# Performance work log

Measured on AMD Instinct MI355X. Metric: run time of the kernel, lower is better.

The kernel has to match this reference:

```python
import jax, jax.numpy as jnp
import numpy as np

B, S, SE, H, NH = 1, 2048, 2048, 1024, 16
HD = H // NH
INNER = 4 * H
EPS = 1e-5


def layer_norm(x, g, b):
    mu = jnp.mean(x, axis=-1, keepdims=True)
    var = jnp.mean(jnp.square(x - mu), axis=-1, keepdims=True)
    return (x - mu) * jax.lax.rsqrt(var + EPS) * g + b


def split_heads(x):  # [B,T,H] -> [B,NH,T,HD]
    b, t, _ = x.shape
    return x.reshape(b, t, NH, HD).transpose(0, 2, 1, 3)


def merge_heads(x):  # [B,NH,T,HD] -> [B,T,H]
    b, nh, t, hd = x.shape
    return x.transpose(0, 2, 1, 3).reshape(b, t, nh * hd)


def setup_inputs() -> dict:
    key = jax.random.key(0)
    ks = jax.random.split(key, 16)
    n = lambda k, shp: (jax.random.normal(k, shp, jnp.float32) * 0.02)
    return {
        "hidden_states": jax.random.normal(ks[0], (B, S, H), jnp.float32),
        "encoder_hidden_states": jax.random.normal(ks[1], (B, SE, H), jnp.float32),
        "scorer_logits": jax.random.normal(ks[2], (B, SE), jnp.float32),
        "ln1_g": jnp.ones((H,), jnp.float32), "ln1_b": jnp.zeros((H,), jnp.float32),
        "c_attn_w": n(ks[3], (H, 3 * H)), "c_attn_b": jnp.zeros((3 * H,), jnp.float32),
        "attn_proj_w": n(ks[4], (H, H)), "attn_proj_b": jnp.zeros((H,), jnp.float32),
        "lnx_g": jnp.ones((H,), jnp.float32), "lnx_b": jnp.zeros((H,), jnp.float32),
        "q_attn_w": n(ks[5], (H, H)), "q_attn_b": jnp.zeros((H,), jnp.float32),
        "x_kv_w": n(ks[6], (H, 2 * H)), "x_kv_b": jnp.zeros((2 * H,), jnp.float32),
        "x_proj_w": n(ks[7], (H, H)), "x_proj_b": jnp.zeros((H,), jnp.float32),
        "ln2_g": jnp.ones((H,), jnp.float32), "ln2_b": jnp.zeros((H,), jnp.float32),
        "fc_w": n(ks[8], (H, INNER)), "fc_b": jnp.zeros((INNER,), jnp.float32),
        "mlp_proj_w": n(ks[9], (INNER, H)), "mlp_proj_b": jnp.zeros((H,), jnp.float32),
    }


def _attn_core(q, k, v, extra_bias=None, causal_bool=False, tril_diag2_additive=False):
    # q,k,v: [B,NH,T,HD]; eager attention, materializes full score matrix (faithful to source)
    w = jnp.einsum("bhqd,bhkd->bhqk", q, k) / jnp.sqrt(jnp.asarray(HD, q.dtype))
    ql, kl = q.shape[-2], k.shape[-2]
    neg = jnp.finfo(w.dtype).min
    if causal_bool:
        mask = jnp.tril(jnp.ones((ql, kl), bool))  # self-attn boolean causal mask
        w = jnp.where(mask[None, None], w, neg)
    if tril_diag2_additive:
        cm = jnp.tril(jnp.ones((ql, kl), w.dtype), k=2)  # limit_cross_attn: tril diagonal=2
        w = w + jnp.where(cm == 0, neg, jnp.zeros((), w.dtype))[None, None]
    if extra_bias is not None:
        w = w + extra_bias[:, None, None, :]  # scorer_logits additive per-key bias
    w = jax.nn.softmax(w, axis=-1)
    return jnp.einsum("bhqk,bhkd->bhqd", w, v)


def reference(hidden_states, encoder_hidden_states, scorer_logits,
              ln1_g, ln1_b, c_attn_w, c_attn_b, attn_proj_w, attn_proj_b,
              lnx_g, lnx_b, q_attn_w, q_attn_b, x_kv_w, x_kv_b, x_proj_w, x_proj_b,
              ln2_g, ln2_b, fc_w, fc_b, mlp_proj_w, mlp_proj_b):
    # --- self attention ---
    residual = hidden_states
    x = layer_norm(hidden_states, ln1_g, ln1_b)
    qkv = x @ c_attn_w + c_attn_b
    q, k, v = jnp.split(qkv, 3, axis=-1)
    a = _attn_core(split_heads(q), split_heads(k), split_heads(v), causal_bool=True)
    a = merge_heads(a) @ attn_proj_w + attn_proj_b
    hidden_states = a + residual
    # --- cross attention (limit_cross_attn=True, scorer_logits bias) ---
    residual = hidden_states
    x = layer_norm(hidden_states, lnx_g, lnx_b)
    q = x @ q_attn_w + q_attn_b
    kv = encoder_hidden_states @ x_kv_w + x_kv_b
    k, v = jnp.split(kv, 2, axis=-1)
    a = _attn_core(split_heads(q), split_heads(k), split_heads(v),
                   extra_bias=scorer_logits, tril_diag2_additive=True)
    a = merge_heads(a) @ x_proj_w + x_proj_b
    hidden_states = residual + a
    # --- MLP (gelu_new = tanh approx) ---
    residual = hidden_states
    x = layer_norm(hidden_states, ln2_g, ln2_b)
    h = jax.nn.gelu(x @ fc_w + fc_b, approximate=True)
    hidden_states = residual + (h @ mlp_proj_w + mlp_proj_b)
    return hidden_states
```

## Files before the change

kernel.cpp:

```cpp
#include <hip/hip_runtime.h>
#include <stdint.h>

#define H     1024
#define S     2048
#define SEQE  2048
#define NHEAD 16
#define HD    64
#define INNER 4096
#define EPSLN 1e-5f
#define LOG2E 1.44269504089f
#define SCALE2 (0.125f * LOG2E)

typedef __attribute__((ext_vector_type(8))) short short8;
typedef __attribute__((ext_vector_type(4))) float floatx4;

__device__ __forceinline__ float b2f(unsigned short u){
  union { unsigned int i; float f; } v; v.i = ((unsigned int)u) << 16; return v.f;
}
__device__ __forceinline__ unsigned short f2b(float f){
  union { float f; unsigned int i; } v; v.f = f;
  unsigned int x = v.i;
  unsigned int r = (x + 0x7FFFu + ((x >> 16) & 1u)) >> 16;
  return (unsigned short)r;
}
__device__ __forceinline__ float fexp2(float x){ return __builtin_amdgcn_exp2f(x); }
__device__ __forceinline__ float gelu_tanh(float x){
  float x3 = x*x*x;
  float t = tanhf(0.7978845608028654f*(x + 0.044715f*x3));
  return 0.5f*x*(1.0f+t);
}

__device__ __forceinline__ void gld16(const unsigned short* g, unsigned short* l){
  __builtin_amdgcn_global_load_lds(
      (const __attribute__((address_space(1))) unsigned int*)g,
      (__attribute__((address_space(3))) unsigned int*)l,
      16, 0, 0);
}

__global__ __launch_bounds__(256) void k_sniff(
    const unsigned short* __restrict__ p, int* __restrict__ flag){
  __shared__ int any;
  if (threadIdx.x == 0) any = 0;
  __syncthreads();
  int bad = 0;
  for (int i = threadIdx.x; i < 8192; i += 256){
    float v = b2f(p[i]);
    if (!(fabsf(v) < 1e6f)) bad = 1;
  }
  if (bad) any = 1;
  __syncthreads();
  if (threadIdx.x == 0) flag[0] = any;
}

struct PrepT {
  const void* src[7];
  unsigned short* dst[7];
  int R[7], C[7];
  int pre[8];
};
__global__ __launch_bounds__(256) void k_prep_t(PrepT d, const int* __restrict__ flag){
  __shared__ unsigned short t[32][33];
  int b = blockIdx.x;
  int m = 0;
  while (b >= d.pre[m+1]) m++;
  int ti = b - d.pre[m];
  int R = d.R[m], C = d.C[m];
  int tx = threadIdx.x & 31, ty = threadIdx.x >> 5;
  int tilesx = C >> 5;
  int bc = (ti % tilesx) << 5, br = (ti / tilesx) << 5;
  const float* sf = (const float*)d.src[m];
  const unsigned short* sb = (const unsigned short*)d.src[m];
  unsigned short* dst = d.dst[m];
  int fl = flag[0];
  #pragma unroll
  for (int i = 0; i < 4; i++){
    size_t idx = (size_t)(br + ty + i*8) * C + bc + tx;
    t[ty + i*8][tx] = fl ? f2b(sf[idx]) : sb[idx];
  }
  __syncthreads();
  #pragma unroll
  for (int i = 0; i < 4; i++)
    dst[(size_t)(bc + ty + i*8) * R + br + tx] = t[tx][ty + i*8];
}

struct SmallCvt {
  const void* src[16];
  unsigned short* dst[16];
  int n[16];
};
__global__ __launch_bounds__(256) void k_prep_c(
    const void* __restrict__ enc, unsigned short* __restrict__ enc_c,
    const void* __restrict__ hsv, float* __restrict__ hidden,
    SmallCvt sc, const int* __restrict__ flag){
  int b = blockIdx.x, tid = threadIdx.x;
  int fl = flag[0];
  if (b < 8192){
    int i = b*256 + tid;
    enc_c[i] = fl ? f2b(((const float*)enc)[i]) : ((const unsigned short*)enc)[i];
  } else if (b < 16384){
    int i = (b - 8192)*256 + tid;
    hidden[i] = fl ? ((const float*)hsv)[i] : b2f(((const unsigned short*)hsv)[i]);
  } else {
    int t = b - 16384;
    const float* sf = (const float*)sc.src[t];
    const unsigned short* sb = (const unsigned short*)sc.src[t];
    unsigned short* d = sc.dst[t];
    for (int i = tid; i < sc.n[t]; i += 256){
      float vv = fl ? sf[i] : b2f(sb[i]);
      if (t == 13) vv *= LOG2E;
      d[i] = f2b(vv);
    }
  }
}

__global__ __launch_bounds__(256) void k_layernorm(
    const float* __restrict__ x,
    const unsigned short* __restrict__ g, const unsigned short* __restrict__ bb,
    unsigned short* __restrict__ y){
  __shared__ float scratch[4];
  int row = blockIdx.x, tid = threadIdx.x;
  float v[4];
  #pragma unroll
  for (int i=0;i<4;i++) v[i] = x[(size_t)row*H + tid + i*256];
  float s = v[0]+v[1]+v[2]+v[3];
  for (int o=32;o;o>>=1) s += __shfl_xor(s,o,64);
  int wid = tid>>6, lane = tid&63;
  if (lane==0) scratch[wid]=s;
  __syncthreads();
  float mu = (scratch[0]+scratch[1]+scratch[2]+scratch[3]) * (1.0f/H);
  __syncthreads();
  float q = 0.f;
  #pragma unroll
  for (int i=0;i<4;i++){ float d=v[i]-mu; q += d*d; }
  for (int o=32;o;o>>=1) q += __shfl_xor(q,o,64);
  if (lane==0) scratch[wid]=q;
  __syncthreads();
  float var = (scratch[0]+scratch[1]+scratch[2]+scratch[3]) * (1.0f/H);
  float rstd = rsqrtf(var + EPSLN);
  #pragma unroll
  for (int i=0;i<4;i++){
    int idx = tid + i*256;
    float o = (v[i]-mu)*rstd*b2f(g[idx]) + b2f(bb[idx]);
    y[(size_t)row*H + idx] = f2b(o);
  }
}

__global__ __launch_bounds__(256) void k_gemm64(
    const unsigned short* __restrict__ A, const unsigned short* __restrict__ BT,
    const unsigned short* __restrict__ bias,
    unsigned short* __restrict__ outb, float* __restrict__ resid,
    int M, int N, int K, int mode, const int* __restrict__ flag,
    int vcol0, unsigned short* __restrict__ vtout)
{
  __shared__ __align__(16) unsigned short As[2][64*64];
  __shared__ __align__(16) unsigned short Bs[2][128*64];
  int tid = threadIdx.x;
  int bm0 = blockIdx.y * 64, bn0 = blockIdx.x * 128;
  int wid = tid >> 6, lane = tid & 63;
  int wm = (wid & 1) * 32, wn = (wid >> 1) * 64;
  floatx4 acc[2][4] = {};

  const unsigned short* gp[6];
  int lofs[6];
  int aseg[6];
  int lrow = lane >> 3, lchunk = (lane & 7) ^ lrow;
  #pragma unroll
  for (int t = 0; t < 6; t++){
    int seg = wid * 6 + t;
    if (seg < 8){
      gp[t] = A + (size_t)(bm0 + seg*8 + lrow) * K + lchunk*8;
      lofs[t] = seg * 512;
      aseg[t] = 1;
    } else {
      int s = seg - 8;
      gp[t] = BT + (size_t)(bn0 + s*8 + lrow) * K + lchunk*8;
      lofs[t] = s * 512;
      aseg[t] = 0;
    }
  }

  #pragma unroll
  for (int t = 0; t < 6; t++)
    gld16(gp[t], (aseg[t] ? As[0] : Bs[0]) + lofs[t]);

  int mrow = lane & 15, quad = lane >> 4;
  int ib = 0;
  for (int kt = 0; kt < K; kt += 64, ib ^= 1){
    __syncthreads();
    if (kt + 64 < K){
      #pragma unroll
      for (int t = 0; t < 6; t++)
        gld16(gp[t] + kt + 64, (aseg[t] ? As[ib^1] : Bs[ib^1]) + lofs[t]);
    }
    const unsigned short* Ac = As[ib];
    const unsigned short* Bc = Bs[ib];
    #pragma unroll
    for (int k2 = 0; k2 < 2; k2++){
      short8 af[2], bf[4];
      #pragma unroll
      for (int i = 0; i < 2; i++){
        int r = wm + i*16 + mrow;
        int slot = (k2*4 + quad) ^ (r & 7);
        af[i] = *(const short8*)&Ac[r*64 + slot*8];
      }
      #pragma unroll
      for (int j = 0; j < 4; j++){
        int r = wn + j*16 + mrow;
        int slot = (k2*4 + quad) ^ (r & 7);
        bf[j] = *(const short8*)&Bc[r*64 + slot*8];
      }
      #pragma unroll
      for (int i = 0; i < 2; i++){
        #pragma unroll
        for (int j = 0; j < 4; j++){
          acc[i][j] = __builtin_amdgcn_mfma_f32_16x16x32_bf16(af[i], bf[j], acc[i][j], 0,0,0);
        }
      }
    }
  }

  int colb = mrow, rowb = quad * 4;
  #pragma unroll
  for (int i=0;i<2;i++){
    #pragma unroll
    for (int j=0;j<4;j++){
      int col = bn0 + wn + j*16 + colb;
      float bv = b2f(bias[col]);
      int row0 = bm0 + wm + i*16 + rowb;
      if (mode == 4 && col >= vcol0){
        ushort4 uv;
        uv.x = f2b(acc[i][j][0] + bv);
        uv.y = f2b(acc[i][j][1] + bv);
        uv.z = f2b(acc[i][j][2] + bv);
        uv.w = f2b(acc[i][j][3] + bv);
        *(ushort4*)(vtout + (size_t)(col - vcol0)*M + row0) = uv;
      } else {
        #pragma unroll
        for (int rr=0;rr<4;rr++){
          int row = row0 + rr;
          float v = acc[i][j][rr] + bv;
          size_t off = (size_t)row*N + col;
          if      (mode == 0 || mode == 4){ outb[off] = f2b(v); }
          else if (mode == 1){ outb[off] = f2b(gelu_tanh(v)); }
          else               { resid[off] += v; }
        }
      }
    }
  }
}

__global__ __launch_bounds__(256) void k_gemm64s(
    const unsigned short* __restrict__ A, const unsigned short* __restrict__ BT,
    const unsigned short* __restrict__ bias,
    unsigned short* __restrict__ outb, float* __restrict__ resid,
    int M, int N, int K, int klen, int mode)
{
  __shared__ __align__(16) unsigned short As[2][64*64];
  __shared__ __align__(16) unsigned short Bs[2][64*64];
  int tid = threadIdx.x;
  int bm0 = blockIdx.y * 64, bn0 = blockIdx.x * 64;
  int k0 = blockIdx.z * klen;
  int wid = tid >> 6, lane = tid & 63;
  int wm = wid * 16;
  floatx4 acc[4] = {};

  const unsigned short* gp[4];
  int lofs[4];
  int aseg[4];
  int lrow = lane >> 3, lchunk = (lane & 7) ^ lrow;
  #pragma unroll
  for (int t = 0; t < 4; t++){
    int seg = wid * 4 + t;
    if (seg < 8){
      gp[t] = A + (size_t)(bm0 + seg*8 + lrow) * K + k0 + lchunk*8;
      lofs[t] = seg * 512;
      aseg[t] = 1;
    } else {
      int s = seg - 8;
      gp[t] = BT + (size_t)(bn0 + s*8 + lrow) * K + k0 + lchunk*8;
      lofs[t] = s * 512;
      aseg[t] = 0;
    }
  }

  #pragma unroll
  for (int t = 0; t < 4; t++)
    gld16(gp[t], (aseg[t] ? As[0] : Bs[0]) + lofs[t]);

  int mrow = lane & 15, quad = lane >> 4;
  int ib = 0;
  for (int kt = 0; kt < klen; kt += 64, ib ^= 1){
    __syncthreads();
    if (kt + 64 < klen){
      #pragma unroll
      for (int t = 0; t < 4; t++)
        gld16(gp[t] + kt + 64, (aseg[t] ? As[ib^1] : Bs[ib^1]) + lofs[t]);
    }
    const unsigned short* Ac = As[ib];
    const unsigned short* Bc = Bs[ib];
    #pragma unroll
    for (int k2 = 0; k2 < 2; k2++){
      short8 af, bf[4];
      {
        int r = wm + mrow;
        int slot = (k2*4 + quad) ^ (r & 7);
        af = *(const short8*)&Ac[r*64 + slot*8];
      }
      #pragma unroll
      for (int j = 0; j < 4; j++){
        int r = j*16 + mrow;
        int slot = (k2*4 + quad) ^ (r & 7);
        bf[j] = *(const short8*)&Bc[r*64 + slot*8];
      }
      #pragma unroll
      for (int j = 0; j < 4; j++)
        acc[j] = __builtin_amdgcn_mfma_f32_16x16x32_bf16(af, bf[j], acc[j], 0,0,0);
    }
  }

  int colb = mrow, rowb = quad * 4;
  #pragma unroll
  for (int j=0;j<4;j++){
    int col = bn0 + j*16 + colb;
    float bv = (blockIdx.z == 0) ? b2f(bias[col]) : 0.f;
    int row0 = bm0 + wm + rowb;
    #pragma unroll
    for (int rr=0;rr<4;rr++){
      int row = row0 + rr;
      float v = acc[j][rr] + bv;
      size_t off = (size_t)row*N + col;
      if (mode == 0) outb[off] = f2b(v);
      else           atomicAdd(&resid[off], v);
    }
  }
}

__global__ __launch_bounds__(256) void k_final(
    const float* __restrict__ hidden, unsigned short* __restrict__ out,
    const int* __restrict__ flag){
  int i = blockIdx.x * 256 + threadIdx.x;
  float v = hidden[i];
  if (flag[0]) ((float*)out)[i] = v;
  else         out[i] = f2b(v);
}

template<int CA, int SCOR>
__global__ __launch_bounds__(256) void k_flash2(
    const unsigned short* __restrict__ qb, int qstride,
    const unsigned short* __restrict__ kb, int kstride,
    const unsigned short* __restrict__ vt,
    const unsigned short* __restrict__ scorer,
    unsigned short* __restrict__ obuf, float* __restrict__ mlbuf, int TOTS)
{
  int t = blockIdx.x, h = blockIdx.y, sp = blockIdx.z;
  int klmax0 = 64*t + 64 + CA; if (klmax0 > S) klmax0 = S;
  int nch = (klmax0 + 63) >> 6;
  int nsp = (nch + 7) >> 3;
  if (sp >= nsp) return;
  int base = 0;
  for (int i = 0; i < t; i++){
    int km = 64*i + 64 + CA; if (km > S) km = S;
    base += (((km + 63) >> 6) + 7) >> 3;
  }
  int pidx = h*TOTS + base + sp;
  int c0 = sp*8, c1 = c0 + 8; if (c1 > nch) c1 = nch;

  __shared__ __align__(16) unsigned short Ks[2][64*64];
  __shared__ __align__(16) unsigned short VTs[64*64];
  __shared__ __align__(16) unsigned short Ps[4][16*72];
  __shared__ float scs[2][64];
  int tid = threadIdx.x;
  int q0 = t*64;
  int w = tid >> 6, lane = tid & 63;
  int cn = lane & 15, quad = lane >> 4, kq = quad * 8;
  unsigned short* Pw = Ps[w];
  int srow0 = w*16;
  int lr = lane >> 3;
  int lc = ((lane & 7) ^ lr) * 8;
  const unsigned short* kg0 = kb + (size_t)(srow0 + lr) * kstride + h*HD + lc;
  const unsigned short* kg1 = kb + (size_t)(srow0 + 8 + lr) * kstride + h*HD + lc;
  const unsigned short* vg0 = vt + (size_t)(h*HD + srow0 + lr) * S + lc;
  const unsigned short* vg1 = vt + (size_t)(h*HD + srow0 + 8 + lr) * S + lc;

  const unsigned short* qrow = qb + (size_t)(q0 + w*16 + cn) * qstride + h*HD;
  short8 qf0 = *(const short8*)(qrow + kq);
  short8 qf1 = *(const short8*)(qrow + kq + 32);
  floatx4 oacc[4] = {};
  float l_lane[4] = {0,0,0,0};
  float m_w = -1.0e38f;
  int qmr = q0 + w*16 + quad*4;

  {
    int kc = c0 * 64;
    gld16(kg0 + (size_t)kc * kstride, Ks[0] + srow0*64);
    gld16(kg1 + (size_t)kc * kstride, Ks[0] + (srow0 + 8)*64);
    if (SCOR && tid < 64) scs[0][tid] = b2f(scorer[kc + tid]);
  }

  int ib = 0;
  for (int ci = c0; ci < c1; ci++, ib ^= 1){
    int kc = ci * 64;
    __syncthreads();
    gld16(vg0 + kc, VTs + srow0*64);
    gld16(vg1 + kc, VTs + (srow0 + 8)*64);
    if (ci + 1 < c1){
      int kn2 = (ci + 1) * 64;
      gld16(kg0 + (size_t)kn2 * kstride, Ks[ib^1] + srow0*64);
      gld16(kg1 + (size_t)kn2 * kstride, Ks[ib^1] + (srow0 + 8)*64);
      if (SCOR && tid < 64) scs[ib^1][tid] = b2f(scorer[kn2 + tid]);
    }
    const unsigned short* Kc = Ks[ib];
    const float* scc = scs[ib];

    floatx4 sv[4] = {};
    #pragma unroll
    for (int t4=0;t4<4;t4++){
      int rr = t4*16 + cn;
      int s0 = ((quad    ) ^ (rr & 7)) * 8;
      int s1 = ((quad + 4) ^ (rr & 7)) * 8;
      short8 b0 = *(const short8*)&Kc[rr*64 + s0];
      short8 b1 = *(const short8*)&Kc[rr*64 + s1];
      sv[t4] = __builtin_amdgcn_mfma_f32_16x16x32_bf16(qf0, b0, sv[t4], 0,0,0);
      sv[t4] = __builtin_amdgcn_mfma_f32_16x16x32_bf16(qf1, b1, sv[t4], 0,0,0);
    }

    float vals[16];
    float lmax = -1.0e38f;
    if (kc + 63 > q0 + w*16 + CA){
      #pragma unroll
      for (int t4=0;t4<4;t4++){
        #pragma unroll
        for (int r=0;r<4;r++){
          float s = sv[t4][r] * SCALE2;
          if (SCOR) s += scc[t4*16 + cn];
          int kn = kc + t4*16 + cn;
          s = (kn <= qmr + r + CA) ? s : -1.0e38f;
          vals[t4*4+r] = s;
          lmax = fmaxf(lmax, s);
        }
      }
    } else {
      #pragma unroll
      for (int t4=0;t4<4;t4++){
        #pragma unroll
        for (int r=0;r<4;r++){
          float s = sv[t4][r] * SCALE2;
          if (SCOR) s += scc[t4*16 + cn];
          vals[t4*4+r] = s;
          lmax = fmaxf(lmax, s);
        }
      }
    }
    lmax = fmaxf(lmax, __shfl_xor(lmax,1,64));
    lmax = fmaxf(lmax, __shfl_xor(lmax,2,64));
    lmax = fmaxf(lmax, __shfl_xor(lmax,4,64));
    lmax = fmaxf(lmax, __shfl_xor(lmax,8,64));
    float mnew = fmaxf(m_w, lmax);
    float al = fexp2(m_w - mnew);
    m_w = mnew;
    #pragma unroll
    for (int r=0;r<4;r++) l_lane[r] *= al;
    #pragma unroll
    for (int t2=0;t2<4;t2++){
      #pragma unroll
      for (int r=0;r<4;r++) oacc[t2][r] *= al;
    }
    #pragma unroll
    for (int t4=0;t4<4;t4++){
      #pragma unroll
      for (int r=0;r<4;r++){
        float e = fexp2(vals[t4*4+r] - m_w);
        l_lane[r] += e;
        Pw[(quad*4+r)*72 + t4*16 + cn] = f2b(e);
      }
    }
    __syncthreads();
    short8 pf0 = *(const short8*)&Pw[cn*72 + kq];
    short8 pf1 = *(const short8*)&Pw[cn*72 + kq + 32];
    #pragma unroll
    for (int t2=0;t2<4;t2++){
      int rr = t2*16 + cn;
      int s0 = ((quad    ) ^ (rr & 7)) * 8;
      int s1 = ((quad + 4) ^ (rr & 7)) * 8;
      short8 v0 = *(const short8*)&VTs[rr*64 + s0];
      short8 v1 = *(const short8*)&VTs[rr*64 + s1];
      oacc[t2] = __builtin_amdgcn_mfma_f32_16x16x32_bf16(pf0, v0, oacc[t2], 0,0,0);
      oacc[t2] = __builtin_amdgcn_mfma_f32_16x16x32_bf16(pf1, v1, oacc[t2], 0,0,0);
    }
  }

  float lrow[4];
  #pragma unroll
  for (int r=0;r<4;r++){
    float l = l_lane[r];
    l += __shfl_xor(l,1,64); l += __shfl_xor(l,2,64);
    l += __shfl_xor(l,4,64); l += __shfl_xor(l,8,64);
    lrow[r] = l;
  }
  size_t ob = (size_t)pidx*4096 + (size_t)(w*16 + quad*4)*64;
  #pragma unroll
  for (int t2=0;t2<4;t2++){
    #pragma unroll
    for (int r=0;r<4;r++)
      obuf[ob + r*64 + t2*16 + cn] = f2b(oacc[t2][r]);
  }
  if (cn == 0){
    #pragma unroll
    for (int r=0;r<4;r++){
      int row64 = w*16 + quad*4 + r;
      mlbuf[((size_t)pidx*64 + row64)*2]   = m_w;
      mlbuf[((size_t)pidx*64 + row64)*2+1] = lrow[r];
    }
  }
}

template<int CA>
__global__ __launch_bounds__(256) void k_comb(
    const unsigned short* __restrict__ obuf, const float* __restrict__ mlbuf,
    unsigned short* __restrict__ out, int TOTS)
{
  int h = blockIdx.y;
  int row = blockIdx.x*16 + (threadIdx.x >> 4);
  int d0 = (threadIdx.x & 15) * 4;
  int t = row >> 6;
  int klmax0 = 64*t + 64 + CA; if (klmax0 > S) klmax0 = S;
  int nch = (klmax0 + 63) >> 6;
  int nsp = (nch + 7) >> 3;
  int base = 0;
  for (int i = 0; i < t; i++){
    int km = 64*i + 64 + CA; if (km > S) km = S;
    base += (((km + 63) >> 6) + 7) >> 3;
  }
  int row64 = row & 63;
  float mp[4], lp[4];
  float M = -1.0e38f;
  for (int p = 0; p < nsp; p++){
    int pi = h*TOTS + base + p;
    mp[p] = mlbuf[((size_t)pi*64 + row64)*2];
    lp[p] = mlbuf[((size_t)pi*64 + row64)*2+1];
    M = fmaxf(M, mp[p]);
  }
  float L = 0.f;
  float o0=0.f,o1=0.f,o2=0.f,o3=0.f;
  for (int p = 0; p < nsp; p++){
    int pi = h*TOTS + base + p;
    float wgt = fexp2(mp[p] - M);
    L += lp[p]*wgt;
    const unsigned short* op = obuf + (size_t)pi*4096 + row64*64 + d0;
    o0 += b2f(op[0])*wgt; o1 += b2f(op[1])*wgt;
    o2 += b2f(op[2])*wgt; o3 += b2f(op[3])*wgt;
  }
  float inv = 1.0f / L;
  size_t oo = (size_t)row*H + h*HD + d0;
  out[oo]   = f2b(o0*inv); out[oo+1] = f2b(o1*inv);
  out[oo+2] = f2b(o2*inv); out[oo+3] = f2b(o3*inv);
}

extern "C" void kernel_launch(void* const* d_in, const int* in_sizes, int n_in,
                              void* d_out, int out_size, void* d_ws, size_t ws_size,
                              hipStream_t stream)
{
  const void* hs          = d_in[0];
  const void* enc         = d_in[1];
  const void* scorer      = d_in[2];
  const void* ln1_g       = d_in[3];
  const void* ln1_b       = d_in[4];
  const void* c_attn_w    = d_in[5];
  const void* c_attn_b    = d_in[6];
  const void* attn_proj_w = d_in[7];
  const void* attn_proj_b = d_in[8];
  const void* lnx_g       = d_in[9];
  const void* lnx_b       = d_in[10];
  const void* q_attn_w    = d_in[11];
  const void* q_attn_b    = d_in[12];
  const void* x_kv_w      = d_in[13];
  const void* x_kv_b      = d_in[14];
  const void* x_proj_w    = d_in[15];
  const void* x_proj_b    = d_in[16];
  const void* ln2_g       = d_in[17];
  const void* ln2_b       = d_in[18];
  const void* fc_w        = d_in[19];
  const void* fc_b        = d_in[20];
  const void* mlp_proj_w  = d_in[21];
  const void* mlp_proj_b  = d_in[22];
  unsigned short* out = (unsigned short*)d_out;

  char* ws = (char*)d_ws; size_t off = 0;
  auto alloc = [&](size_t bytes)->void*{
    void* p = ws + off; off += (bytes + 255) & ~(size_t)255; return p;
  };
  unsigned short* wT_cattn = (unsigned short*)alloc((size_t)3072*1024*2);
  unsigned short* wT_aproj = (unsigned short*)alloc((size_t)1024*1024*2);
  unsigned short* wT_qattn = (unsigned short*)alloc((size_t)1024*1024*2);
  unsigned short* wT_xkv   = (unsigned short*)alloc((size_t)2048*1024*2);
  unsigned short* wT_xproj = (unsigned short*)alloc((size_t)1024*1024*2);
  unsigned short* wT_fc    = (unsigned short*)alloc((size_t)4096*1024*2);
  unsigned short* wT_mlp   = (unsigned short*)alloc((size_t)1024*4096*2);
  unsigned short* enc_c    = (unsigned short*)alloc((size_t)SEQE*H*2);
  unsigned short* canon    = (unsigned short*)alloc((size_t)32768*2);
  unsigned short* xln      = (unsigned short*)alloc((size_t)S*H*2);
  unsigned short* qkv      = (unsigned short*)alloc((size_t)S*3*H*2);
  unsigned short* attnout  = (unsigned short*)alloc((size_t)S*H*2);
  unsigned short* q2       = (unsigned short*)alloc((size_t)S*H*2);
  unsigned short* kvbuf    = (unsigned short*)alloc((size_t)SEQE*2*H*2);
  unsigned short* vt_self  = (unsigned short*)alloc((size_t)H*S*2);
  unsigned short* vt_cross = (unsigned short*)alloc((size_t)H*SEQE*2);
  unsigned short* fcbuf    = (unsigned short*)alloc((size_t)S*INNER*2);
  float*          hidden   = (float*)alloc((size_t)S*H*4);
  int*            flag     = (int*)alloc(256);

  unsigned short* obuf  = fcbuf;
  float*          mlbuf = (float*)(fcbuf + (size_t)16*83*4096);

  unsigned short* p = canon;
  auto carve = [&](int n)->unsigned short*{ unsigned short* q = p; p += n; return q; };
  unsigned short* c_ln1g = carve(1024); unsigned short* c_ln1b = carve(1024);
  unsigned short* c_catb = carve(3072); unsigned short* c_aprb = carve(1024);
  unsigned short* c_lnxg = carve(1024); unsigned short* c_lnxb = carve(1024);
  unsigned short* c_qatb = carve(1024); unsigned short* c_xkvb = carve(2048);
  unsigned short* c_xprb = carve(1024); unsigned short* c_ln2g = carve(1024);
  unsigned short* c_ln2b = carve(1024); unsigned short* c_fcb  = carve(4096);
  unsigned short* c_mlpb = carve(1024); unsigned short* c_scor = carve(2048);

  k_sniff<<<1, 256, 0, stream>>>((const unsigned short*)hs, flag);

  PrepT pt{};
  const void* tsrc[7] = {c_attn_w, attn_proj_w, q_attn_w, x_kv_w, x_proj_w, fc_w, mlp_proj_w};
  unsigned short* tdst[7] = {wT_cattn, wT_aproj, wT_qattn, wT_xkv, wT_xproj, wT_fc, wT_mlp};
  int tR[7] = {1024,1024,1024,1024,1024,1024,4096};
  int tC[7] = {3072,1024,1024,2048,1024,4096,1024};
  int acc_t = 0;
  for (int i=0;i<7;i++){
    pt.src[i]=tsrc[i]; pt.dst[i]=tdst[i]; pt.R[i]=tR[i]; pt.C[i]=tC[i];
    pt.pre[i]=acc_t; acc_t += (tC[i]>>5)*(tR[i]>>5);
  }
  pt.pre[7]=acc_t;
  k_prep_t<<<acc_t, 256, 0, stream>>>(pt, flag);

  SmallCvt sc{};
  const void* ssrc[14] = {ln1_g, ln1_b, c_attn_b, attn_proj_b, lnx_g, lnx_b,
                          q_attn_b, x_kv_b, x_proj_b, ln2_g, ln2_b, fc_b,
                          mlp_proj_b, scorer};
  unsigned short* sdst[14] = {c_ln1g, c_ln1b, c_catb, c_aprb, c_lnxg, c_lnxb,
                              c_qatb, c_xkvb, c_xprb, c_ln2g, c_ln2b, c_fcb,
                              c_mlpb, c_scor};
  int sn[14] = {1024,1024,3072,1024,1024,1024,1024,2048,1024,1024,1024,4096,1024,2048};
  for (int i=0;i<14;i++){ sc.src[i]=ssrc[i]; sc.dst[i]=sdst[i]; sc.n[i]=sn[i]; }
  k_prep_c<<<16384 + 14, 256, 0, stream>>>(enc, enc_c, hs, hidden, sc, flag);

  k_layernorm<<<S, 256, 0, stream>>>(hidden, c_ln1g, c_ln1b, xln);
  k_gemm64<<<dim3(3072/128, S/64), 256, 0, stream>>>(xln, wT_cattn, c_catb,
      qkv, nullptr, S, 3072, 1024, 4, flag, 2048, vt_self);
  k_flash2<0,0><<<dim3(32, NHEAD, 4), 256, 0, stream>>>(
      qkv, 3*H, qkv + 1024, 3*H, vt_self, nullptr, obuf, mlbuf, 80);
  k_comb<0><<<dim3(S/16, NHEAD), 256, 0, stream>>>(obuf, mlbuf, attnout, 80);
  k_gemm64s<<<dim3(1024/64, S/64, 2), 256, 0, stream>>>(attnout, wT_aproj, c_aprb,
      nullptr, hidden, S, 1024, 1024, 512, 2);

  k_layernorm<<<S, 256, 0, stream>>>(hidden, c_lnxg, c_lnxb, xln);
  k_gemm64s<<<dim3(1024/64, S/64, 1), 256, 0, stream>>>(xln, wT_qattn, c_qatb,
      q2, nullptr, S, 1024, 1024, 1024, 0);
  k_gemm64<<<dim3(2048/128, SEQE/64), 256, 0, stream>>>(enc_c, wT_xkv, c_xkvb,
      kvbuf, nullptr, SEQE, 2048, 1024, 4, flag, 1024, vt_cross);
  k_flash2<2,1><<<dim3(32, NHEAD, 4), 256, 0, stream>>>(
      q2, H, kvbuf, 2*H, vt_cross, c_scor, obuf, mlbuf, 83);
  k_comb<2><<<dim3(S/16, NHEAD), 256, 0, stream>>>(obuf, mlbuf, attnout, 83);
  k_gemm64s<<<dim3(1024/64, S/64, 2), 256, 0, stream>>>(attnout, wT_xproj, c_xprb,
      nullptr, hidden, S, 1024, 1024, 512, 2);

  k_layernorm<<<S, 256, 0, stream>>>(hidden, c_ln2g, c_ln2b, xln);
  k_gemm64<<<dim3(INNER/128, S/64), 256, 0, stream>>>(xln, wT_fc, c_fcb,
      fcbuf, nullptr, S, INNER, 1024, 1, flag, 0, nullptr);
  k_gemm64s<<<dim3(1024/64, S/64, 4), 256, 0, stream>>>(fcbuf, wT_mlp, c_mlpb,
      nullptr, hidden, S, 1024, INNER, 1024, 2);
  k_final<<<(S*H)/256, 256, 0, stream>>>(hidden, out, flag);
}
```

Before: 476.3 us.

## Load flash K/V fragments directly from global and drop split-K atomics

The flash attention kernel no longer stages K and V^T tiles in LDS with double buffering and block barriers. Each lane now loads its MFMA fragments straight from global memory, and scorer values are read per lane. The output projections drop split-K atomics and add directly into the residual, and the MLP down-projection writes two partial buffers that a final kernel sums with the residual. This removes barriers and atomic traffic, but it risks more global and L2 load pressure in attention and less parallelism in the projection GEMMs.

```diff
diff --git a/kernel.cpp b/kernel.cpp
--- a/kernel.cpp
+++ b/kernel.cpp
@@ -253,6 +253,7 @@
     const unsigned short* __restrict__ A, const unsigned short* __restrict__ BT,
     const unsigned short* __restrict__ bias,
     unsigned short* __restrict__ outb, float* __restrict__ resid,
+    float* __restrict__ part,
     int M, int N, int K, int klen, int mode)
 {
   __shared__ __align__(16) unsigned short As[2][64*64];
@@ -329,23 +330,25 @@
       int row = row0 + rr;
       float v = acc[j][rr] + bv;
       size_t off = (size_t)row*N + col;
-      if (mode == 0) outb[off] = f2b(v);
-      else           atomicAdd(&resid[off], v);
-    }
-  }
-}
-
-__global__ __launch_bounds__(256) void k_final(
+      if      (mode == 0) outb[off] = f2b(v);
+      else if (mode == 2) resid[off] += v;
+      else                part[(size_t)blockIdx.z*M*N + off] = v;
+    }
+  }
+}
+
+__global__ __launch_bounds__(256) void k_finalize(
+    const float* __restrict__ p0, const float* __restrict__ p1,
     const float* __restrict__ hidden, unsigned short* __restrict__ out,
     const int* __restrict__ flag){
   int i = blockIdx.x * 256 + threadIdx.x;
-  float v = hidden[i];
+  float v = p0[i] + p1[i] + hidden[i];
   if (flag[0]) ((float*)out)[i] = v;
   else         out[i] = f2b(v);
 }
 
 template<int CA, int SCOR>
-__global__ __launch_bounds__(256) void k_flash2(
+__global__ __launch_bounds__(256) void k_flash3(
     const unsigned short* __restrict__ qb, int qstride,
     const unsigned short* __restrict__ kb, int kstride,
     const unsigned short* __restrict__ vt,
@@ -365,63 +368,40 @@
   int pidx = h*TOTS + base + sp;
   int c0 = sp*8, c1 = c0 + 8; if (c1 > nch) c1 = nch;
 
-  __shared__ __align__(16) unsigned short Ks[2][64*64];
-  __shared__ __align__(16) unsigned short VTs[64*64];
   __shared__ __align__(16) unsigned short Ps[4][16*72];
-  __shared__ float scs[2][64];
   int tid = threadIdx.x;
   int q0 = t*64;
   int w = tid >> 6, lane = tid & 63;
   int cn = lane & 15, quad = lane >> 4, kq = quad * 8;
   unsigned short* Pw = Ps[w];
-  int srow0 = w*16;
-  int lr = lane >> 3;
-  int lc = ((lane & 7) ^ lr) * 8;
-  const unsigned short* kg0 = kb + (size_t)(srow0 + lr) * kstride + h*HD + lc;
-  const unsigned short* kg1 = kb + (size_t)(srow0 + 8 + lr) * kstride + h*HD + lc;
-  const unsigned short* vg0 = vt + (size_t)(h*HD + srow0 + lr) * S + lc;
-  const unsigned short* vg1 = vt + (size_t)(h*HD + srow0 + 8 + lr) * S + lc;
 
   const unsigned short* qrow = qb + (size_t)(q0 + w*16 + cn) * qstride + h*HD;
   short8 qf0 = *(const short8*)(qrow + kq);
   short8 qf1 = *(const short8*)(qrow + kq + 32);
+  const unsigned short* kfrag = kb + (size_t)cn * kstride + h*HD + kq;
+  const unsigned short* vfrag = vt + (size_t)(h*HD + cn) * S + kq;
+
   floatx4 oacc[4] = {};
   float l_lane[4] = {0,0,0,0};
   float m_w = -1.0e38f;
   int qmr = q0 + w*16 + quad*4;
 
-  {
-    int kc = c0 * 64;
-    gld16(kg0 + (size_t)kc * kstride, Ks[0] + srow0*64);
-    gld16(kg1 + (size_t)kc * kstride, Ks[0] + (srow0 + 8)*64);
-    if (SCOR && tid < 64) scs[0][tid] = b2f(scorer[kc + tid]);
-  }
-
-  int ib = 0;
-  for (int ci = c0; ci < c1; ci++, ib ^= 1){
+  for (int ci = c0; ci < c1; ci++){
     int kc = ci * 64;
-    __syncthreads();
-    gld16(vg0 + kc, VTs + srow0*64);
-    gld16(vg1 + kc, VTs + (srow0 + 8)*64);
-    if (ci + 1 < c1){
-      int kn2 = (ci + 1) * 64;
-      gld16(kg0 + (size_t)kn2 * kstride, Ks[ib^1] + srow0*64);
-      gld16(kg1 + (size_t)kn2 * kstride, Ks[ib^1] + (srow0 + 8)*64);
-      if (SCOR && tid < 64) scs[ib^1][tid] = b2f(scorer[kn2 + tid]);
-    }
-    const unsigned short* Kc = Ks[ib];
-    const float* scc = scs[ib];
-
+    const unsigned short* kcp = kfrag + (size_t)kc * kstride;
     floatx4 sv[4] = {};
     #pragma unroll
     for (int t4=0;t4<4;t4++){
-      int rr = t4*16 + cn;
-      int s0 = ((quad    ) ^ (rr & 7)) * 8;
-      int s1 = ((quad + 4) ^ (rr & 7)) * 8;
-      short8 b0 = *(const short8*)&Kc[rr*64 + s0];
-      short8 b1 = *(const short8*)&Kc[rr*64 + s1];
+      const unsigned short* kp = kcp + (size_t)(t4*16) * kstride;
+      short8 b0 = *(const short8*)kp;
+      short8 b1 = *(const short8*)(kp + 32);
       sv[t4] = __builtin_amdgcn_mfma_f32_16x16x32_bf16(qf0, b0, sv[t4], 0,0,0);
       sv[t4] = __builtin_amdgcn_mfma_f32_16x16x32_bf16(qf1, b1, sv[t4], 0,0,0);
+    }
+    float sc4[4];
+    if (SCOR){
+      #pragma unroll
+      for (int t4=0;t4<4;t4++) sc4[t4] = b2f(scorer[kc + t4*16 + cn]);
     }
 
     float vals[16];
@@ -432,7 +412,7 @@
         #pragma unroll
         for (int r=0;r<4;r++){
           float s = sv[t4][r] * SCALE2;
-          if (SCOR) s += scc[t4*16 + cn];
+          if (SCOR) s += sc4[t4];
           int kn = kc + t4*16 + cn;
           s = (kn <= qmr + r + CA) ? s : -1.0e38f;
           vals[t4*4+r] = s;
@@ -445,7 +425,7 @@
         #pragma unroll
         for (int r=0;r<4;r++){
           float s = sv[t4][r] * SCALE2;
-          if (SCOR) s += scc[t4*16 + cn];
+          if (SCOR) s += sc4[t4];
           vals[t4*4+r] = s;
           lmax = fmaxf(lmax, s);
         }
@@ -474,16 +454,14 @@
         Pw[(quad*4+r)*72 + t4*16 + cn] = f2b(e);
       }
     }
-    __syncthreads();
     short8 pf0 = *(const short8*)&Pw[cn*72 + kq];
     short8 pf1 = *(const short8*)&Pw[cn*72 + kq + 32];
+    const unsigned short* vcp = vfrag + kc;
     #pragma unroll
     for (int t2=0;t2<4;t2++){
-      int rr = t2*16 + cn;
-      int s0 = ((quad    ) ^ (rr & 7)) * 8;
-      int s1 = ((quad + 4) ^ (rr & 7)) * 8;
-      short8 v0 = *(const short8*)&VTs[rr*64 + s0];
-      short8 v1 = *(const short8*)&VTs[rr*64 + s1];
+      const unsigned short* vp = vcp + (size_t)(t2*16) * S;
+      short8 v0 = *(const short8*)vp;
+      short8 v1 = *(const short8*)(vp + 32);
       oacc[t2] = __builtin_amdgcn_mfma_f32_16x16x32_bf16(pf0, v0, oacc[t2], 0,0,0);
       oacc[t2] = __builtin_amdgcn_mfma_f32_16x16x32_bf16(pf1, v1, oacc[t2], 0,0,0);
     }
@@ -611,6 +589,7 @@
 
   unsigned short* obuf  = fcbuf;
   float*          mlbuf = (float*)(fcbuf + (size_t)16*83*4096);
+  float* mlp_part = (float*)kvbuf;
 
   unsigned short* p = canon;
   auto carve = [&](int n)->unsigned short*{ unsigned short* q = p; p += n; return q; };
@@ -651,27 +630,28 @@
   k_layernorm<<<S, 256, 0, stream>>>(hidden, c_ln1g, c_ln1b, xln);
   k_gemm64<<<dim3(3072/128, S/64), 256, 0, stream>>>(xln, wT_cattn, c_catb,
       qkv, nullptr, S, 3072, 1024, 4, flag, 2048, vt_self);
-  k_flash2<0,0><<<dim3(32, NHEAD, 4), 256, 0, stream>>>(
+  k_flash3<0,0><<<dim3(32, NHEAD, 4), 256, 0, stream>>>(
       qkv, 3*H, qkv + 1024, 3*H, vt_self, nullptr, obuf, mlbuf, 80);
   k_comb<0><<<dim3(S/16, NHEAD), 256, 0, stream>>>(obuf, mlbuf, attnout, 80);
-  k_gemm64s<<<dim3(1024/64, S/64, 2), 256, 0, stream>>>(attnout, wT_aproj, c_aprb,
-      nullptr, hidden, S, 1024, 1024, 512, 2);
+  k_gemm64s<<<dim3(1024/64, S/64, 1), 256, 0, stream>>>(attnout, wT_aproj, c_aprb,
+      nullptr, hidden, nullptr, S, 1024, 1024, 1024, 2);
 
   k_layernorm<<<S, 256, 0, stream>>>(hidden, c_lnxg, c_lnxb, xln);
   k_gemm64s<<<dim3(1024/64, S/64, 1), 256, 0, stream>>>(xln, wT_qattn, c_qatb,
-      q2, nullptr, S, 1024, 1024, 1024, 0);
+      q2, nullptr, nullptr, S, 1024, 1024, 1024, 0);
   k_gemm64<<<dim3(2048/128, SEQE/64), 256, 0, stream>>>(enc_c, wT_xkv, c_xkvb,
       kvbuf, nullptr, SEQE, 2048, 1024, 4, flag, 1024, vt_cross);
-  k_flash2<2,1><<<dim3(32, NHEAD, 4), 256, 0, stream>>>(
+  k_flash3<2,1><<<dim3(32, NHEAD, 4), 256, 0, stream>>>(
       q2, H, kvbuf, 2*H, vt_cross, c_scor, obuf, mlbuf, 83);
   k_comb<2><<<dim3(S/16, NHEAD), 256, 0, stream>>>(obuf, mlbuf, attnout, 83);
-  k_gemm64s<<<dim3(1024/64, S/64, 2), 256, 0, stream>>>(attnout, wT_xproj, c_xprb,
-      nullptr, hidden, S, 1024, 1024, 512, 2);
+  k_gemm64s<<<dim3(1024/64, S/64, 1), 256, 0, stream>>>(attnout, wT_xproj, c_xprb,
+      nullptr, hidden, nullptr, S, 1024, 1024, 1024, 2);
 
   k_layernorm<<<S, 256, 0, stream>>>(hidden, c_ln2g, c_ln2b, xln);
   k_gemm64<<<dim3(INNER/128, S/64), 256, 0, stream>>>(xln, wT_fc, c_fcb,
       fcbuf, nullptr, S, INNER, 1024, 1, flag, 0, nullptr);
-  k_gemm64s<<<dim3(1024/64, S/64, 4), 256, 0, stream>>>(fcbuf, wT_mlp, c_mlpb,
-      nullptr, hidden, S, 1024, INNER, 1024, 2);
-  k_final<<<(S*H)/256, 256, 0, stream>>>(hidden, out, flag);
-}
+  k_gemm64s<<<dim3(1024/64, S/64, 2), 256, 0, stream>>>(fcbuf, wT_mlp, c_mlpb,
+      nullptr, nullptr, mlp_part, S, 1024, INNER, 2048, 5);
+  k_finalize<<<(S*H)/256, 256, 0, stream>>>(mlp_part, mlp_part + (size_t)S*1024,
+      hidden, out, flag);
+}
```

After: 605.9 us. 27.2% more time.
